# Kernel tuning notes

Hardware: AMD Instinct MI355X
Metric: run time of the kernel (lower is better)

Reference implementation:

```python
import jax, jax.numpy as jnp
import numpy as np
from jax import lax

B, T, H = 128, 512, 512


def _lstm_cell(x, h, c, Wih, Whh, bih, bhh):
    # PyTorch LSTMCell: gates = x@Wih.T + bih + h@Whh.T + bhh; order i,f,g,o
    gates = x @ Wih.T + h @ Whh.T + (bih + bhh)
    i, f, g, o = jnp.split(gates, 4, axis=-1)
    i = jax.nn.sigmoid(i)
    f = jax.nn.sigmoid(f)
    g = jnp.tanh(g)
    o = jax.nn.sigmoid(o)
    c_new = f * c + i * g
    h_new = o * jnp.tanh(c_new)
    return h_new, c_new


def setup_inputs() -> dict:
    key = jax.random.key(0)
    ks = jax.random.split(key, 20)
    s = 1.0 / np.sqrt(H)
    u = lambda k, shape: jax.random.uniform(k, shape, jnp.float32, -s, s)
    d = {
        "x": jax.random.normal(ks[0], (B, T), jnp.float32),
        "future": 0,
        "W1": u(ks[1], (H, 1)), "b1": u(ks[2], (H,)),
        "W2": u(ks[3], (1, H)), "b2": u(ks[4], (1,)),
    }
    i = 5
    for l in (1, 2, 3):
        d[f"Wih{l}"] = u(ks[i], (4 * H, H)); i += 1
        d[f"Whh{l}"] = u(ks[i], (4 * H, H)); i += 1
        d[f"bih{l}"] = u(ks[i], (4 * H,)); i += 1
        d[f"bhh{l}"] = u(ks[i], (4 * H,)); i += 1
    return d


def reference(x, future, W1, b1, W2, b2,
              Wih1, Whh1, bih1, bhh1,
              Wih2, Whh2, bih2, bhh2,
              Wih3, Whh3, bih3, bhh3):
    Bx = x.shape[0]
    Hd = W1.shape[0]
    zero = jnp.zeros((Bx, Hd), x.dtype)

    def stack_step(carry, xp):  # xp: [B, H] projected input
        h1, c1, h2, c2, h3, c3 = carry
        h1, c1 = _lstm_cell(xp, h1, c1, Wih1, Whh1, bih1, bhh1)
        h2, c2 = _lstm_cell(h1, h2, c2, Wih2, Whh2, bih2, bhh2)
        h3, c3 = _lstm_cell(h2, h3, c3, Wih3, Whh3, bih3, bhh3)
        out = h3 @ W2.T + b2  # [B, 1]
        return (h1, c1, h2, c2, h3, c3), out[:, 0]

    def scan_step(carry, xt):  # xt: [B] scalar input per step
        xp = xt[:, None] * W1[:, 0][None, :] + b1  # linear1 on [B,1]
        return stack_step(carry, xp)

    carry = (zero, zero, zero, zero, zero, zero)
    carry, outs = lax.scan(scan_step, carry, x.T)  # outs: [T, B]
    outputs = outs.T  # [B, T]

    if future > 0:
        out = outputs[:, -1]
        extra = []
        for _ in range(future):
            xp = out[:, None] * W1[:, 0][None, :] + b1
            carry, out = stack_step(carry, xp)
            extra.append(out)
        outputs = jnp.concatenate([outputs, jnp.stack(extra, axis=1)], axis=1)
    return outputs
```

## Files before the change

### kernel.cpp

```cpp
#include <hip/hip_runtime.h>

typedef short short8 __attribute__((ext_vector_type(8)));
typedef float f32x4  __attribute__((ext_vector_type(4)));
typedef unsigned long long u64;

#define NSTEP 515

#define OFF_WH1  0ull
#define OFF_WH2  2097152ull
#define OFF_WH3  4194304ull
#define OFF_WI2  6291456ull
#define OFF_WI3  8388608ull
#define OFF_V1   10485760ull
#define OFF_U1   10493952ull
#define OFF_B2   10502144ull
#define OFF_B3   10510336ull
#define OFF_XT   10518528ull
#define OFF_HR   10780672ull
#define OFF_P3   11567104ull
#define OFF_C    11616256ull

__device__ __forceinline__ unsigned short bf16rne(float f) {
    unsigned u = __float_as_uint(f);
    return (unsigned short)((u + 0x7FFFu + ((u >> 16) & 1u)) >> 16);
}

__device__ __forceinline__ float sigm(float x) { return 1.0f / (1.0f + expf(-x)); }

__global__ void fill_sentinel(float* __restrict__ out)
{
    int e = blockIdx.x * 256 + threadIdx.x;
    if (e < 65536) out[e] = 0.75f;
}

__global__ void zero_state(char* __restrict__ ws)
{
    int e = blockIdx.x * 256 + threadIdx.x;
    float4 z = {0.f, 0.f, 0.f, 0.f};
    if (e < 101376) *(float4*)(ws + OFF_HR + (size_t)e * 16) = z;
}

__global__ void pack_w(const float* __restrict__ W, unsigned short* __restrict__ dst)
{
    int e = blockIdx.x * 256 + threadIdx.x;
    int j    = e & 7;
    int lane = (e >> 3) & 63;
    int nb   = (e >> 9) & 3;
    int kb   = (e >> 11) & 15;
    int ug   = e >> 15;
    int row = nb * 512 + ug * 16 + (lane & 15);
    int col = kb * 32 + (lane >> 4) * 8 + j;
    dst[e] = bf16rne(W[row * 512 + col]);
}

__global__ void prep_vec(const float* __restrict__ Wih1, const float* __restrict__ W1,
                         const float* __restrict__ b1,
                         const float* __restrict__ bih1, const float* __restrict__ bhh1,
                         const float* __restrict__ bih2, const float* __restrict__ bhh2,
                         const float* __restrict__ bih3, const float* __restrict__ bhh3,
                         float* __restrict__ v1, float* __restrict__ u1,
                         float* __restrict__ bias2, float* __restrict__ bias3)
{
    int r = blockIdx.x * 256 + threadIdx.x;
    if (r >= 2048) return;
    float sv = 0.f, su = 0.f;
    for (int k = 0; k < 512; ++k) {
        float w = Wih1[r * 512 + k];
        sv += w * W1[k];
        su += w * b1[k];
    }
    v1[r] = sv;
    u1[r] = su + bih1[r] + bhh1[r];
    bias2[r] = bih2[r] + bhh2[r];
    bias3[r] = bih3[r] + bhh3[r];
}

__global__ void prep_xt(const float* __restrict__ x, float* __restrict__ xT)
{
    int e = blockIdx.x * 256 + threadIdx.x;
    if (e >= 65536) return;
    int b = e >> 9, t = e & 511;
    xT[t * 128 + b] = x[e];
}

template<int NM>
__device__ __forceinline__ void gemm_chunks(
    const unsigned short* __restrict__ wsrc0,
    const unsigned short* __restrict__ wsrc1,
    const short8 (&A)[NM][16],
    unsigned short (&bsh)[2][8192],
    int tid, int lane, f32x4 (&acc)[4])
{
    const unsigned short* wsrc[2] = { wsrc0, wsrc1 };
    short8 r0, r1;
    r0 = *(const short8*)(wsrc[0] + tid * 8);
    r1 = *(const short8*)(wsrc[0] + 4096 + tid * 8);
    *(short8*)(&bsh[0][tid * 8]) = r0;
    *(short8*)(&bsh[0][4096 + tid * 8]) = r1;
    __syncthreads();
    #pragma unroll
    for (int cc = 0; cc < 4 * NM; ++cc) {
        const int m = cc >> 2, c = cc & 3;
        const int nm_ = cc + 1;
        if (nm_ < 4 * NM) {
            const unsigned short* src = wsrc[nm_ >> 2] + (nm_ & 3) * 8192;
            r0 = *(const short8*)(src + tid * 8);
            r1 = *(const short8*)(src + 4096 + tid * 8);
        }
        (void)c;
        #pragma unroll
        for (int k2 = 0; k2 < 4; ++k2) {
            const int kb = (cc & 3) * 4 + k2;
            #pragma unroll
            for (int nb = 0; nb < 4; ++nb) {
                short8 bw = *(const short8*)(&bsh[cc & 1][(k2 * 4 + nb) * 512 + lane * 8]);
                acc[nb] = __builtin_amdgcn_mfma_f32_16x16x32_bf16(A[m][kb], bw, acc[nb], 0, 0, 0);
            }
        }
        if (nm_ < 4 * NM) {
            *(short8*)(&bsh[nm_ & 1][tid * 8]) = r0;
            *(short8*)(&bsh[nm_ & 1][4096 + tid * 8]) = r1;
        }
        __syncthreads();
    }
}

__global__ void __launch_bounds__(512)
step_k(char* __restrict__ ws, const float* __restrict__ W2,
       const float* __restrict__ b2, float* __restrict__ out, int w)
{
    __shared__ __align__(16) unsigned short bsh[2][8192];
    __shared__ __align__(16) unsigned short stage[8][16][16];

    const int cur = w & 1, prev = cur ^ 1;
    const int tid = threadIdx.x, lane = tid & 63, wv = tid >> 6;
    const int q = lane >> 4, l15 = lane & 15;
    const int wg = blockIdx.x;

    unsigned short* hr = (unsigned short*)(ws + OFF_HR);
    float* part3 = (float*)(ws + OFF_P3);

    if (wg == 96) {
        if (w < 3 || tid >= 128) return;
        const int b = tid;
        const float* p = part3 + (size_t)((w - 1) % 3) * 32 * 128;
        float v = 0.f;
        #pragma unroll
        for (int i = 0; i < 32; ++i) v += p[i * 128 + b];
        out[(size_t)b * 512 + (w - 3)] = v + b2[0];
        return;
    }

    const int layer = wg >> 5, ug = wg & 31;
    const int t = w - layer;
    if (t < 0 || t >= 512) return;
    const int gu = ug * 16 + l15;

    float cv[4], cu_[4];
    if (layer == 0) {
        const float* v1 = (const float*)(ws + OFF_V1);
        const float* u1 = (const float*)(ws + OFF_U1);
        #pragma unroll
        for (int g = 0; g < 4; ++g) { cv[g] = v1[g * 512 + gu]; cu_[g] = u1[g * 512 + gu]; }
    } else {
        const float* bs = (const float*)(ws + ((layer == 1) ? OFF_B2 : OFF_B3));
        #pragma unroll
        for (int g = 0; g < 4; ++g) { cv[g] = bs[g * 512 + gu]; cu_[g] = 0.f; }
    }
    const float w2v = (layer == 2) ? W2[gu] : 0.f;
    const float* xT = (const float*)(ws + OFF_XT);
    float* C = (float*)(ws + OFF_C);

    float c_st[4];
    #pragma unroll
    for (int rr = 0; rr < 4; ++rr) {
        const int b = wv * 16 + q * 4 + rr;
        c_st[rr] = C[((size_t)layer * 128 + b) * 512 + gu];
    }

    f32x4 acc[4] = {};
    if (layer == 0) {
        const unsigned short* hS = hr + (size_t)(0 * 2 + prev) * 65536;
        short8 A[1][16];
        #pragma unroll
        for (int kb = 0; kb < 16; ++kb)
            A[0][kb] = *(const short8*)(hS + ((kb * 8 + wv) * 512) + lane * 8);
        gemm_chunks<1>((const unsigned short*)(ws + OFF_WH1) + (size_t)ug * 32768,
                       nullptr, A, bsh, tid, lane, acc);
    } else {
        const unsigned short* hA0 = hr + (size_t)((layer - 1) * 2 + prev) * 65536;
        const unsigned short* hA1 = hr + (size_t)(layer * 2 + prev) * 65536;
        short8 A[2][16];
        #pragma unroll
        for (int kb = 0; kb < 16; ++kb)
            A[0][kb] = *(const short8*)(hA0 + ((kb * 8 + wv) * 512) + lane * 8);
        #pragma unroll
        for (int kb = 0; kb < 16; ++kb)
            A[1][kb] = *(const short8*)(hA1 + ((kb * 8 + wv) * 512) + lane * 8);
        gemm_chunks<2>((const unsigned short*)(ws + ((layer == 1) ? OFF_WI2 : OFF_WI3)) + (size_t)ug * 32768,
                       (const unsigned short*)(ws + ((layer == 1) ? OFF_WH2 : OFF_WH3)) + (size_t)ug * 32768,
                       A, bsh, tid, lane, acc);
    }

    #pragma unroll
    for (int rr = 0; rr < 4; ++rr) {
        const int b = wv * 16 + q * 4 + rr;
        const float xv = (layer == 0) ? xT[t * 128 + b] : 1.0f;
        float gi = acc[0][rr] + xv * cv[0] + cu_[0];
        float gf = acc[1][rr] + xv * cv[1] + cu_[1];
        float gg = acc[2][rr] + xv * cv[2] + cu_[2];
        float go = acc[3][rr] + xv * cv[3] + cu_[3];
        float c = sigm(gf) * c_st[rr] + sigm(gi) * tanhf(gg);
        C[((size_t)layer * 128 + b) * 512 + gu] = c;
        float h = sigm(go) * tanhf(c);
        stage[wv][q * 4 + rr][l15] = bf16rne(h);
        if (layer == 2) {
            float v = h * w2v;
            v += __shfl_xor(v, 1); v += __shfl_xor(v, 2);
            v += __shfl_xor(v, 4); v += __shfl_xor(v, 8);
            if (l15 == 0)
                part3[((size_t)(w % 3) * 32 + ug) * 128 + b] = v;
        }
    }
    {
        u64* dst64 = (u64*)(hr + (size_t)(layer * 2 + cur) * 65536
                               + ((size_t)(ug >> 1) * 8 + wv) * 512);
        const int row = lane >> 2, q4 = lane & 3;
        u64 v = *(const u64*)&stage[wv][row][q4 * 4];
        const int idx = (((ug & 1) * 2 + (q4 >> 1)) * 16 + row) * 2 + (q4 & 1);
        dst64[idx] = v;
    }
}

__global__ void Sequence_85564338471528_kernel() {}

extern "C" void kernel_launch(void* const* d_in, const int* in_sizes, int n_in,
                              void* d_out, int out_size, void* d_ws, size_t ws_size,
                              hipStream_t stream)
{
    const float* x    = (const float*)d_in[0];
    const float* W1   = (const float*)d_in[2];
    const float* b1   = (const float*)d_in[3];
    const float* W2   = (const float*)d_in[4];
    const float* b2   = (const float*)d_in[5];
    const float* Wih1 = (const float*)d_in[6];
    const float* Whh1 = (const float*)d_in[7];
    const float* bih1 = (const float*)d_in[8];
    const float* bhh1 = (const float*)d_in[9];
    const float* Wih2 = (const float*)d_in[10];
    const float* Whh2 = (const float*)d_in[11];
    const float* bih2 = (const float*)d_in[12];
    const float* bhh2 = (const float*)d_in[13];
    const float* Wih3 = (const float*)d_in[14];
    const float* Whh3 = (const float*)d_in[15];
    const float* bih3 = (const float*)d_in[16];
    const float* bhh3 = (const float*)d_in[17];
    char* ws = (char*)d_ws;
    float* out = (float*)d_out;

    fill_sentinel<<<256, 256, 0, stream>>>(out);
    zero_state<<<396, 256, 0, stream>>>(ws);

    pack_w<<<4096, 256, 0, stream>>>(Whh1, (unsigned short*)(ws + OFF_WH1));
    pack_w<<<4096, 256, 0, stream>>>(Whh2, (unsigned short*)(ws + OFF_WH2));
    pack_w<<<4096, 256, 0, stream>>>(Whh3, (unsigned short*)(ws + OFF_WH3));
    pack_w<<<4096, 256, 0, stream>>>(Wih2, (unsigned short*)(ws + OFF_WI2));
    pack_w<<<4096, 256, 0, stream>>>(Wih3, (unsigned short*)(ws + OFF_WI3));
    prep_vec<<<8, 256, 0, stream>>>(Wih1, W1, b1, bih1, bhh1, bih2, bhh2, bih3, bhh3,
                                    (float*)(ws + OFF_V1), (float*)(ws + OFF_U1),
                                    (float*)(ws + OFF_B2), (float*)(ws + OFF_B3));
    prep_xt<<<256, 256, 0, stream>>>(x, (float*)(ws + OFF_XT));

    for (int w = 0; w < NSTEP; ++w)
        step_k<<<97, 512, 0, stream>>>(ws, W2, b2, out, w);
}
```

Baseline: 5.873 ms.

## Fuse two wavefront steps per launch with a hierarchical grid barrier

Each launch now processes two consecutive wavefront steps. A software grid barrier uses grouped atomic counters and coherent loads and stores between the two steps, so the number of kernel launches is halved. Cell state stays in registers between the two steps, which saves one global round trip of C per pair. This trades launch overhead for atomic barrier spinning and cache-bypassing loads, and it depends on all 97 workgroups being resident at the same time.

Result: no change. 5.975 ms (+1.7%).

```diff
diff --git a/kernel.cpp b/kernel.cpp
--- a/kernel.cpp
+++ b/kernel.cpp
@@ -5,6 +5,10 @@
 typedef unsigned long long u64;
 
 #define NSTEP 515
+#define NDISP 258
+#define NWG 96
+#define NGRP 8
+#define GSZ  12
 
 #define OFF_WH1  0ull
 #define OFF_WH2  2097152ull
@@ -19,6 +23,7 @@
 #define OFF_HR   10780672ull
 #define OFF_P3   11567104ull
 #define OFF_C    11616256ull
+#define OFF_BAR  12402688ull
 
 __device__ __forceinline__ unsigned short bf16rne(float f) {
     unsigned u = __float_as_uint(f);
@@ -27,6 +32,21 @@
 
 __device__ __forceinline__ float sigm(float x) { return 1.0f / (1.0f + expf(-x)); }
 
+__device__ __forceinline__ short8 cload16(const void* p) {
+    short8 r;
+    asm volatile("global_load_dwordx4 %0, %1, off sc0 sc1" : "=v"(r) : "v"(p));
+    return r;
+}
+__device__ __forceinline__ float cload4(const void* p) {
+    float r;
+    asm volatile("global_load_dword %0, %1, off sc0 sc1" : "=v"(r) : "v"(p));
+    return r;
+}
+__device__ __forceinline__ void vm_drain() {
+    asm volatile("s_waitcnt vmcnt(0)" ::: "memory");
+    __builtin_amdgcn_sched_barrier(0);
+}
+
 __global__ void fill_sentinel(float* __restrict__ out)
 {
     int e = blockIdx.x * 256 + threadIdx.x;
@@ -38,6 +58,11 @@
     int e = blockIdx.x * 256 + threadIdx.x;
     float4 z = {0.f, 0.f, 0.f, 0.f};
     if (e < 101376) *(float4*)(ws + OFF_HR + (size_t)e * 16) = z;
+}
+
+__global__ void zero_bar(char* __restrict__ ws)
+{
+    ((unsigned*)(ws + OFF_BAR))[threadIdx.x] = 0u;
 }
 
 __global__ void pack_w(const float* __restrict__ W, unsigned short* __restrict__ dst)
@@ -83,6 +108,30 @@
     xT[t * 128 + b] = x[e];
 }
 
+__device__ __forceinline__ void gbar_arrive(unsigned* bar, int wg, unsigned s)
+{
+    __syncthreads();
+    if (threadIdx.x == 0) {
+        unsigned g = (unsigned)wg & 7u;
+        unsigned old = atomicAdd(bar + 64 + g * 32, 1u);
+        if (old == s * GSZ - 1) {
+            unsigned ro = atomicAdd(bar, 1u);
+            if (ro == s * NGRP - 1)
+                __hip_atomic_store(bar + 32, s, __ATOMIC_RELAXED,
+                                   __HIP_MEMORY_SCOPE_AGENT);
+        }
+    }
+}
+__device__ __forceinline__ void gbar_wait(unsigned* bar, unsigned s)
+{
+    if (threadIdx.x == 0) {
+        while (__hip_atomic_load(bar + 32, __ATOMIC_RELAXED,
+                                 __HIP_MEMORY_SCOPE_AGENT) < s)
+            __builtin_amdgcn_s_sleep(1);
+    }
+    __syncthreads();
+}
+
 template<int NM>
 __device__ __forceinline__ void gemm_chunks(
     const unsigned short* __restrict__ wsrc0,
@@ -100,14 +149,13 @@
     __syncthreads();
     #pragma unroll
     for (int cc = 0; cc < 4 * NM; ++cc) {
-        const int m = cc >> 2, c = cc & 3;
+        const int m = cc >> 2;
         const int nm_ = cc + 1;
         if (nm_ < 4 * NM) {
             const unsigned short* src = wsrc[nm_ >> 2] + (nm_ & 3) * 8192;
             r0 = *(const short8*)(src + tid * 8);
             r1 = *(const short8*)(src + 4096 + tid * 8);
         }
-        (void)c;
         #pragma unroll
         for (int k2 = 0; k2 < 4; ++k2) {
             const int kb = (cc & 3) * 4 + k2;
@@ -125,36 +173,130 @@
     }
 }
 
+template<int COH>
+__device__ __forceinline__ void load_A16(short8 (&A)[16], const unsigned short* h,
+                                         int wv, int lane)
+{
+    #pragma unroll
+    for (int kb = 0; kb < 16; ++kb) {
+        const void* p = h + ((kb * 8 + wv) * 512) + lane * 8;
+        if constexpr (COH) A[kb] = cload16(p);
+        else               A[kb] = *(const short8*)p;
+    }
+}
+
+template<int INC, int OUTC>
+__device__ __forceinline__ void lstm_body(
+    char* __restrict__ ws, unsigned short* __restrict__ hr, float* __restrict__ part3,
+    const float* __restrict__ xT, int w, int layer, int ug,
+    int tid, int lane, int wv, int q, int l15, int gu,
+    const float (&cv)[4], const float (&cu_)[4], float w2v,
+    float (&c_st)[4],
+    unsigned short (&bsh)[2][8192], unsigned short (&stage)[8][16][16])
+{
+    const int cur = w & 1, prev = cur ^ 1;
+    const int t = w - layer;
+    if (t < 0 || t >= 512) return;
+
+    f32x4 acc[4] = {};
+    if (layer == 0) {
+        short8 A[1][16];
+        load_A16<INC>(A[0], hr + (size_t)prev * 65536, wv, lane);
+        if constexpr (INC) vm_drain();
+        gemm_chunks<1>((const unsigned short*)(ws + OFF_WH1) + (size_t)ug * 32768,
+                       nullptr, A, bsh, tid, lane, acc);
+    } else {
+        short8 A[2][16];
+        load_A16<INC>(A[0], hr + (size_t)((layer - 1) * 2 + prev) * 65536, wv, lane);
+        load_A16<INC>(A[1], hr + (size_t)(layer * 2 + prev) * 65536, wv, lane);
+        if constexpr (INC) vm_drain();
+        gemm_chunks<2>((const unsigned short*)(ws + ((layer == 1) ? OFF_WI2 : OFF_WI3)) + (size_t)ug * 32768,
+                       (const unsigned short*)(ws + ((layer == 1) ? OFF_WH2 : OFF_WH3)) + (size_t)ug * 32768,
+                       A, bsh, tid, lane, acc);
+    }
+
+    #pragma unroll
+    for (int rr = 0; rr < 4; ++rr) {
+        const int b = wv * 16 + q * 4 + rr;
+        const float xv = (layer == 0) ? xT[t * 128 + b] : 1.0f;
+        float gi = acc[0][rr] + xv * cv[0] + cu_[0];
+        float gf = acc[1][rr] + xv * cv[1] + cu_[1];
+        float gg = acc[2][rr] + xv * cv[2] + cu_[2];
+        float go = acc[3][rr] + xv * cv[3] + cu_[3];
+        float c = sigm(gf) * c_st[rr] + sigm(gi) * tanhf(gg);
+        c_st[rr] = c;
+        float h = sigm(go) * tanhf(c);
+        stage[wv][q * 4 + rr][l15] = bf16rne(h);
+        if (layer == 2) {
+            float v = h * w2v;
+            v += __shfl_xor(v, 1); v += __shfl_xor(v, 2);
+            v += __shfl_xor(v, 4); v += __shfl_xor(v, 8);
+            if (l15 == 0) {
+                float* p = &part3[((size_t)(w % 3) * 32 + ug) * 128 + b];
+                if constexpr (OUTC)
+                    __hip_atomic_store(p, v, __ATOMIC_RELAXED, __HIP_MEMORY_SCOPE_AGENT);
+                else
+                    *p = v;
+            }
+        }
+    }
+    {
+        u64* dst64 = (u64*)(hr + (size_t)(layer * 2 + cur) * 65536
+                               + ((size_t)(ug >> 1) * 8 + wv) * 512);
+        const int row = lane >> 2, q4 = lane & 3;
+        u64 v = *(const u64*)&stage[wv][row][q4 * 4];
+        const int idx = (((ug & 1) * 2 + (q4 >> 1)) * 16 + row) * 2 + (q4 & 1);
+        if constexpr (OUTC)
+            __hip_atomic_store(dst64 + idx, v, __ATOMIC_RELAXED, __HIP_MEMORY_SCOPE_AGENT);
+        else
+            dst64[idx] = v;
+    }
+}
+
 __global__ void __launch_bounds__(512)
-step_k(char* __restrict__ ws, const float* __restrict__ W2,
-       const float* __restrict__ b2, float* __restrict__ out, int w)
+step2_k(char* __restrict__ ws, const float* __restrict__ W2,
+        const float* __restrict__ b2, float* __restrict__ out, int j)
 {
     __shared__ __align__(16) unsigned short bsh[2][8192];
     __shared__ __align__(16) unsigned short stage[8][16][16];
 
-    const int cur = w & 1, prev = cur ^ 1;
     const int tid = threadIdx.x, lane = tid & 63, wv = tid >> 6;
     const int q = lane >> 4, l15 = lane & 15;
     const int wg = blockIdx.x;
+    const int wA = 2 * j, wB = 2 * j + 1;
+    const unsigned s = (unsigned)j + 1;
 
     unsigned short* hr = (unsigned short*)(ws + OFF_HR);
     float* part3 = (float*)(ws + OFF_P3);
+    unsigned* bar = (unsigned*)(ws + OFF_BAR);
 
     if (wg == 96) {
-        if (w < 3 || tid >= 128) return;
-        const int b = tid;
-        const float* p = part3 + (size_t)((w - 1) % 3) * 32 * 128;
-        float v = 0.f;
-        #pragma unroll
-        for (int i = 0; i < 32; ++i) v += p[i * 128 + b];
-        out[(size_t)b * 512 + (w - 3)] = v + b2[0];
+        if (wA >= 3 && tid < 128) {
+            const float* p = part3 + (size_t)((wA - 1) % 3) * 32 * 128;
+            float v = 0.f;
+            #pragma unroll
+            for (int i = 0; i < 32; ++i) v += p[i * 128 + tid];
+            out[(size_t)tid * 512 + (wA - 3)] = v + b2[0];
+        }
+        gbar_wait(bar, s);
+        if (wB >= 3 && wB < 515 && tid < 128) {
+            const float* p = part3 + (size_t)((wB - 1) % 3) * 32 * 128;
+            float vv[32];
+            #pragma unroll
+            for (int i = 0; i < 32; ++i) vv[i] = cload4(p + i * 128 + tid);
+            vm_drain();
+            float v = 0.f;
+            #pragma unroll
+            for (int i = 0; i < 32; ++i) v += vv[i];
+            out[(size_t)tid * 512 + (wB - 3)] = v + b2[0];
+        }
         return;
     }
 
     const int layer = wg >> 5, ug = wg & 31;
-    const int t = w - layer;
-    if (t < 0 || t >= 512) return;
     const int gu = ug * 16 + l15;
+    const float* xT = (const float*)(ws + OFF_XT);
+    float* C = (float*)(ws + OFF_C);
 
     float cv[4], cu_[4];
     if (layer == 0) {
@@ -168,8 +310,6 @@
         for (int g = 0; g < 4; ++g) { cv[g] = bs[g * 512 + gu]; cu_[g] = 0.f; }
     }
     const float w2v = (layer == 2) ? W2[gu] : 0.f;
-    const float* xT = (const float*)(ws + OFF_XT);
-    float* C = (float*)(ws + OFF_C);
 
     float c_st[4];
     #pragma unroll
@@ -178,57 +318,17 @@
         c_st[rr] = C[((size_t)layer * 128 + b) * 512 + gu];
     }
 
-    f32x4 acc[4] = {};
-    if (layer == 0) {
-        const unsigned short* hS = hr + (size_t)(0 * 2 + prev) * 65536;
-        short8 A[1][16];
-        #pragma unroll
-        for (int kb = 0; kb < 16; ++kb)
-            A[0][kb] = *(const short8*)(hS + ((kb * 8 + wv) * 512) + lane * 8);
-        gemm_chunks<1>((const unsigned short*)(ws + OFF_WH1) + (size_t)ug * 32768,
-                       nullptr, A, bsh, tid, lane, acc);
-    } else {
-        const unsigned short* hA0 = hr + (size_t)((layer - 1) * 2 + prev) * 65536;
-        const unsigned short* hA1 = hr + (size_t)(layer * 2 + prev) * 65536;
-        short8 A[2][16];
-        #pragma unroll
-        for (int kb = 0; kb < 16; ++kb)
-            A[0][kb] = *(const short8*)(hA0 + ((kb * 8 + wv) * 512) + lane * 8);
-        #pragma unroll
-        for (int kb = 0; kb < 16; ++kb)
-            A[1][kb] = *(const short8*)(hA1 + ((kb * 8 + wv) * 512) + lane * 8);
-        gemm_chunks<2>((const unsigned short*)(ws + ((layer == 1) ? OFF_WI2 : OFF_WI3)) + (size_t)ug * 32768,
-                       (const unsigned short*)(ws + ((layer == 1) ? OFF_WH2 : OFF_WH3)) + (size_t)ug * 32768,
-                       A, bsh, tid, lane, acc);
-    }
+    lstm_body<0, 1>(ws, hr, part3, xT, wA, layer, ug, tid, lane, wv, q, l15, gu,
+                    cv, cu_, w2v, c_st, bsh, stage);
+    gbar_arrive(bar, wg, s);
+    gbar_wait(bar, s);
+    lstm_body<1, 0>(ws, hr, part3, xT, wB, layer, ug, tid, lane, wv, q, l15, gu,
+                    cv, cu_, w2v, c_st, bsh, stage);
 
     #pragma unroll
     for (int rr = 0; rr < 4; ++rr) {
         const int b = wv * 16 + q * 4 + rr;
-        const float xv = (layer == 0) ? xT[t * 128 + b] : 1.0f;
-        float gi = acc[0][rr] + xv * cv[0] + cu_[0];
-        float gf = acc[1][rr] + xv * cv[1] + cu_[1];
-        float gg = acc[2][rr] + xv * cv[2] + cu_[2];
-        float go = acc[3][rr] + xv * cv[3] + cu_[3];
-        float c = sigm(gf) * c_st[rr] + sigm(gi) * tanhf(gg);
-        C[((size_t)layer * 128 + b) * 512 + gu] = c;
-        float h = sigm(go) * tanhf(c);
-        stage[wv][q * 4 + rr][l15] = bf16rne(h);
-        if (layer == 2) {
-            float v = h * w2v;
-            v += __shfl_xor(v, 1); v += __shfl_xor(v, 2);
-            v += __shfl_xor(v, 4); v += __shfl_xor(v, 8);
-            if (l15 == 0)
-                part3[((size_t)(w % 3) * 32 + ug) * 128 + b] = v;
-        }
-    }
-    {
-        u64* dst64 = (u64*)(hr + (size_t)(layer * 2 + cur) * 65536
-                               + ((size_t)(ug >> 1) * 8 + wv) * 512);
-        const int row = lane >> 2, q4 = lane & 3;
-        u64 v = *(const u64*)&stage[wv][row][q4 * 4];
-        const int idx = (((ug & 1) * 2 + (q4 >> 1)) * 16 + row) * 2 + (q4 & 1);
-        dst64[idx] = v;
+        C[((size_t)layer * 128 + b) * 512 + gu] = c_st[rr];
     }
 }
 
@@ -260,6 +360,7 @@
 
     fill_sentinel<<<256, 256, 0, stream>>>(out);
     zero_state<<<396, 256, 0, stream>>>(ws);
+    zero_bar<<<1, 1024, 0, stream>>>(ws);
 
     pack_w<<<4096, 256, 0, stream>>>(Whh1, (unsigned short*)(ws + OFF_WH1));
     pack_w<<<4096, 256, 0, stream>>>(Whh2, (unsigned short*)(ws + OFF_WH2));
@@ -271,6 +372,6 @@
                                     (float*)(ws + OFF_B2), (float*)(ws + OFF_B3));
     prep_xt<<<256, 256, 0, stream>>>(x, (float*)(ws + OFF_XT));
 
-    for (int w = 0; w < NSTEP; ++w)
-        step_k<<<97, 512, 0, stream>>>(ws, W2, b2, out, w);
-}
+    for (int j = 0; j < NDISP; ++j)
+        step2_k<<<97, 512, 0, stream>>>(ws, W2, b2, out, j);
+}
```

## Split batch across two workgroups per unit group and load full weight tile into LDS

Applied to the files above, without the earlier changes.

The per-step kernel now launches 193 workgroups of 256 threads instead of 97 of 512. Each (layer, unit-group) pair is split into two batch halves, so more CUs take part in each timestep. The chunked double-buffered weight streaming is replaced by loading the whole 64KB weight tile into dynamic LDS at once and then running all MFMAs. The LDS staging of h is replaced with direct scattered 2-byte global stores. Weights are read twice as often from L2 overall, and the single large LDS load gives up the old overlap between loads and compute.

Result: faster. 4.880 ms (-16.9%).

```diff
diff --git a/kernel.cpp b/kernel.cpp
--- a/kernel.cpp
+++ b/kernel.cpp
@@ -84,53 +84,45 @@
 }
 
 template<int NM>
-__device__ __forceinline__ void gemm_chunks(
+__device__ __forceinline__ void gemm_full(
     const unsigned short* __restrict__ wsrc0,
     const unsigned short* __restrict__ wsrc1,
     const short8 (&A)[NM][16],
-    unsigned short (&bsh)[2][8192],
+    unsigned short* __restrict__ bsh,
     int tid, int lane, f32x4 (&acc)[4])
 {
-    const unsigned short* wsrc[2] = { wsrc0, wsrc1 };
-    short8 r0, r1;
-    r0 = *(const short8*)(wsrc[0] + tid * 8);
-    r1 = *(const short8*)(wsrc[0] + 4096 + tid * 8);
-    *(short8*)(&bsh[0][tid * 8]) = r0;
-    *(short8*)(&bsh[0][4096 + tid * 8]) = r1;
-    __syncthreads();
+    const unsigned short* ws2[2] = { wsrc0, wsrc1 };
     #pragma unroll
-    for (int cc = 0; cc < 4 * NM; ++cc) {
-        const int m = cc >> 2, c = cc & 3;
-        const int nm_ = cc + 1;
-        if (nm_ < 4 * NM) {
-            const unsigned short* src = wsrc[nm_ >> 2] + (nm_ & 3) * 8192;
-            r0 = *(const short8*)(src + tid * 8);
-            r1 = *(const short8*)(src + 4096 + tid * 8);
+    for (int m = 0; m < NM; ++m) {
+        if (m) __syncthreads();
+        short8 br[8];
+        #pragma unroll
+        for (int g = 0; g < 2; ++g) {
+            #pragma unroll
+            for (int i = 0; i < 8; ++i)
+                br[i] = *(const short8*)(ws2[m] + (g * 8 + i) * 2048 + tid * 8);
+            #pragma unroll
+            for (int i = 0; i < 8; ++i)
+                *(short8*)(bsh + (g * 8 + i) * 2048 + tid * 8) = br[i];
         }
-        (void)c;
-        #pragma unroll
-        for (int k2 = 0; k2 < 4; ++k2) {
-            const int kb = (cc & 3) * 4 + k2;
+        __syncthreads();
+        #pragma unroll
+        for (int kb = 0; kb < 16; ++kb) {
             #pragma unroll
             for (int nb = 0; nb < 4; ++nb) {
-                short8 bw = *(const short8*)(&bsh[cc & 1][(k2 * 4 + nb) * 512 + lane * 8]);
+                short8 bw = *(const short8*)(bsh + (kb * 4 + nb) * 512 + lane * 8);
                 acc[nb] = __builtin_amdgcn_mfma_f32_16x16x32_bf16(A[m][kb], bw, acc[nb], 0, 0, 0);
             }
         }
-        if (nm_ < 4 * NM) {
-            *(short8*)(&bsh[nm_ & 1][tid * 8]) = r0;
-            *(short8*)(&bsh[nm_ & 1][4096 + tid * 8]) = r1;
-        }
-        __syncthreads();
-    }
-}
-
-__global__ void __launch_bounds__(512)
+    }
+}
+
+__global__ void __launch_bounds__(256)
 step_k(char* __restrict__ ws, const float* __restrict__ W2,
        const float* __restrict__ b2, float* __restrict__ out, int w)
 {
-    __shared__ __align__(16) unsigned short bsh[2][8192];
-    __shared__ __align__(16) unsigned short stage[8][16][16];
+    extern __shared__ char ldsraw[];
+    unsigned short* bsh = (unsigned short*)ldsraw;
 
     const int cur = w & 1, prev = cur ^ 1;
     const int tid = threadIdx.x, lane = tid & 63, wv = tid >> 6;
@@ -140,7 +132,7 @@
     unsigned short* hr = (unsigned short*)(ws + OFF_HR);
     float* part3 = (float*)(ws + OFF_P3);
 
-    if (wg == 96) {
+    if (wg == 192) {
         if (w < 3 || tid >= 128) return;
         const int b = tid;
         const float* p = part3 + (size_t)((w - 1) % 3) * 32 * 128;
@@ -151,10 +143,12 @@
         return;
     }
 
-    const int layer = wg >> 5, ug = wg & 31;
+    const int bh = wg / 96, lw = wg % 96;
+    const int layer = lw >> 5, ug = lw & 31;
     const int t = w - layer;
     if (t < 0 || t >= 512) return;
     const int gu = ug * 16 + l15;
+    const int mblk = bh * 4 + wv;
 
     float cv[4], cu_[4];
     if (layer == 0) {
@@ -174,37 +168,40 @@
     float c_st[4];
     #pragma unroll
     for (int rr = 0; rr < 4; ++rr) {
-        const int b = wv * 16 + q * 4 + rr;
+        const int b = mblk * 16 + q * 4 + rr;
         c_st[rr] = C[((size_t)layer * 128 + b) * 512 + gu];
     }
 
     f32x4 acc[4] = {};
     if (layer == 0) {
-        const unsigned short* hS = hr + (size_t)(0 * 2 + prev) * 65536;
+        const unsigned short* hS = hr + (size_t)prev * 65536;
         short8 A[1][16];
         #pragma unroll
         for (int kb = 0; kb < 16; ++kb)
-            A[0][kb] = *(const short8*)(hS + ((kb * 8 + wv) * 512) + lane * 8);
-        gemm_chunks<1>((const unsigned short*)(ws + OFF_WH1) + (size_t)ug * 32768,
-                       nullptr, A, bsh, tid, lane, acc);
+            A[0][kb] = *(const short8*)(hS + ((kb * 8 + mblk) * 512) + lane * 8);
+        gemm_full<1>((const unsigned short*)(ws + OFF_WH1) + (size_t)ug * 32768,
+                     nullptr, A, bsh, tid, lane, acc);
     } else {
         const unsigned short* hA0 = hr + (size_t)((layer - 1) * 2 + prev) * 65536;
         const unsigned short* hA1 = hr + (size_t)(layer * 2 + prev) * 65536;
         short8 A[2][16];
         #pragma unroll
         for (int kb = 0; kb < 16; ++kb)
-            A[0][kb] = *(const short8*)(hA0 + ((kb * 8 + wv) * 512) + lane * 8);
+            A[0][kb] = *(const short8*)(hA0 + ((kb * 8 + mblk) * 512) + lane * 8);
         #pragma unroll
         for (int kb = 0; kb < 16; ++kb)
-            A[1][kb] = *(const short8*)(hA1 + ((kb * 8 + wv) * 512) + lane * 8);
-        gemm_chunks<2>((const unsigned short*)(ws + ((layer == 1) ? OFF_WI2 : OFF_WI3)) + (size_t)ug * 32768,
-                       (const unsigned short*)(ws + ((layer == 1) ? OFF_WH2 : OFF_WH3)) + (size_t)ug * 32768,
-                       A, bsh, tid, lane, acc);
-    }
-
+            A[1][kb] = *(const short8*)(hA1 + ((kb * 8 + mblk) * 512) + lane * 8);
+        gemm_full<2>((const unsigned short*)(ws + ((layer == 1) ? OFF_WI2 : OFF_WI3)) + (size_t)ug * 32768,
+                     (const unsigned short*)(ws + ((layer == 1) ? OFF_WH2 : OFF_WH3)) + (size_t)ug * 32768,
+                     A, bsh, tid, lane, acc);
+    }
+
+    const int u5 = (ug & 1) * 16 + l15;
+    unsigned short* dblk = hr + (size_t)(layer * 2 + cur) * 65536
+                              + ((size_t)(ug >> 1) * 8 + mblk) * 512;
     #pragma unroll
     for (int rr = 0; rr < 4; ++rr) {
-        const int b = wv * 16 + q * 4 + rr;
+        const int b = mblk * 16 + q * 4 + rr;
         const float xv = (layer == 0) ? xT[t * 128 + b] : 1.0f;
         float gi = acc[0][rr] + xv * cv[0] + cu_[0];
         float gf = acc[1][rr] + xv * cv[1] + cu_[1];
@@ -213,7 +210,7 @@
         float c = sigm(gf) * c_st[rr] + sigm(gi) * tanhf(gg);
         C[((size_t)layer * 128 + b) * 512 + gu] = c;
         float h = sigm(go) * tanhf(c);
-        stage[wv][q * 4 + rr][l15] = bf16rne(h);
+        dblk[((u5 >> 3) * 16 + (q * 4 + rr)) * 8 + (u5 & 7)] = bf16rne(h);
         if (layer == 2) {
             float v = h * w2v;
             v += __shfl_xor(v, 1); v += __shfl_xor(v, 2);
@@ -221,14 +218,6 @@
             if (l15 == 0)
                 part3[((size_t)(w % 3) * 32 + ug) * 128 + b] = v;
         }
-    }
-    {
-        u64* dst64 = (u64*)(hr + (size_t)(layer * 2 + cur) * 65536
-                               + ((size_t)(ug >> 1) * 8 + wv) * 512);
-        const int row = lane >> 2, q4 = lane & 3;
-        u64 v = *(const u64*)&stage[wv][row][q4 * 4];
-        const int idx = (((ug & 1) * 2 + (q4 >> 1)) * 16 + row) * 2 + (q4 & 1);
-        dst64[idx] = v;
     }
 }
 
@@ -272,5 +261,5 @@
     prep_xt<<<256, 256, 0, stream>>>(x, (float*)(ws + OFF_XT));
 
     for (int w = 0; w < NSTEP; ++w)
-        step_k<<<97, 512, 0, stream>>>(ws, W2, b2, out, w);
-}
+        step_k<<<193, 256, 65536, stream>>>(ws, W2, b2, out, w);
+}
```
